# Kernel optimization log

Hardware: AMD Instinct MI355X
Metric: run time of the kernel (lower is better)

Reference implementation:

```python
import jax, jax.numpy as jnp
import numpy as np

# ---- static config (mirrors init_kwargs) ----
B, A, NC = 16, 3, 80          # batch, anchors-per-head, classes
W = H = 76                     # grid (inputwidth / stride-8)
INPUTW = 608.0
M = 32                         # GT boxes per image
IGNORE = 0.5                   # ignore_thresh
MASK_N = 3                     # mask = [0,1,2] -> first 3 anchors belong to this head
ANCHORS = np.array([[10,13],[16,30],[33,23],[30,61],[62,45],[59,119],
                    [116,90],[156,198],[373,326]], dtype=np.float32)


def _box_iou(b1, b2):
    """b1 [N,4], b2 [P,4] xyxy -> iou [N,P] (same math as torch box_iou)."""
    area1 = (b1[:, 2] - b1[:, 0]) * (b1[:, 3] - b1[:, 1])
    area2 = (b2[:, 2] - b2[:, 0]) * (b2[:, 3] - b2[:, 1])
    lt = jnp.maximum(b1[:, None, :2], b2[None, :, :2])
    rb = jnp.minimum(b1[:, None, 2:], b2[None, :, 2:])
    inter = jnp.clip(rb - lt, 0.0).prod(-1)
    return inter / (area1[:, None] + area2[None, :] - inter)


def setup_inputs() -> dict:
    key = jax.random.key(0)
    k1, k2, k3, k4 = jax.random.split(key, 4)
    prediction = jax.random.normal(k1, (B, A * (5 + NC), W, H), jnp.float32) * 0.5
    # gt rows: (label, cx, cy, w, h, batch_idx), normalized coords, sorted by image
    labels = jax.random.randint(k2, (B * M, 1), 0, NC).astype(jnp.float32)
    cxy = jax.random.uniform(k3, (B * M, 2), minval=0.15, maxval=0.85)
    wh = jax.random.uniform(k4, (B * M, 2), minval=0.05, maxval=0.30)
    bidx = jnp.repeat(jnp.arange(B, dtype=jnp.float32), M)[:, None]
    gt = jnp.concatenate([labels, cxy, wh, bidx], axis=1)
    return {"prediction": prediction, "gt": gt}


def reference(prediction, gt):
    p = prediction.reshape(B, A, W, H, 5 + NC)
    cxp = jax.nn.sigmoid(p[..., 0])
    cyp = jax.nn.sigmoid(p[..., 1])
    wp, hp = p[..., 2], p[..., 3]
    confp = jax.nn.sigmoid(p[..., 4])
    classesp = jax.nn.sigmoid(p[..., 5:])
    # decode (anchors_g are the ORIGINAL pixel anchors: assigned before /strides)
    aw = jnp.asarray(ANCHORS[:MASK_N, 0]).reshape(1, A, 1, 1)
    ah = jnp.asarray(ANCHORS[:MASK_N, 1]).reshape(1, A, 1, 1)
    predx = cxp + jnp.arange(W, dtype=p.dtype)[None, None, None, :]
    predy = cyp + jnp.arange(H, dtype=p.dtype)[None, None, :, None]
    predw = jnp.exp(wp) * aw / INPUTW * W
    predh = jnp.exp(hp) * ah / INPUTW * H
    decoded = jnp.concatenate([predx[..., None], predy[..., None], predw[..., None],
                               predh[..., None], confp[..., None], classesp], axis=-1)

    # predicted boxes in pixel xyxy, flattened per image: [B, A*W*H, 4]
    x1 = (predx - predw * 0.5) / W * INPUTW
    y1 = (predy - predh * 0.5) / H * INPUTW
    x2 = (predx + predw * 0.5) / W * INPUTW
    y2 = (predy + predh * 0.5) / H * INPUTW
    pr = jnp.stack([x1, y1, x2, y2], axis=-1).reshape(B, -1, 4)

    # GT boxes per image (fixed M per image, rows sorted by batch idx)
    gtb = gt.reshape(B, M, 6)
    cx, cy, gw, gh = gtb[..., 1], gtb[..., 2], gtb[..., 3], gtb[..., 4]
    gxyxy = jnp.stack([(cx - gw * 0.5) * INPUTW, (cy - gh * 0.5) * INPUTW,
                       (cx + gw * 0.5) * INPUTW, (cy + gh * 0.5) * INPUTW], axis=-1)

    # per-image GT x all-preds IoU; noobj where best IoU <= ignore_thresh
    iou = jax.vmap(_box_iou)(gxyxy, pr)            # [B, M, A*W*H]
    maxv = iou.max(axis=1).reshape(B, A, H, W)      # W==H so flat order matches
    noobj = maxv <= IGNORE

    # best-anchor assignment per GT (vs all 9 anchors centered at the GT)
    ori = jnp.asarray(ANCHORS) / INPUTW             # [9,2] normalized
    fcx, fcy = cx.reshape(-1), cy.reshape(-1)       # [B*M]
    gflat = gxyxy.reshape(-1, 4)
    abox = jnp.stack([(fcx[:, None] - ori[None, :, 0] * 0.5) * INPUTW,
                      (fcy[:, None] - ori[None, :, 1] * 0.5) * INPUTW,
                      (fcx[:, None] + ori[None, :, 0] * 0.5) * INPUTW,
                      (fcy[:, None] + ori[None, :, 1] * 0.5) * INPUTW], axis=-1)  # [BM,9,4]
    lt = jnp.maximum(gflat[:, None, :2], abox[..., :2])
    rb = jnp.minimum(gflat[:, None, 2:], abox[..., 2:])
    inter = jnp.clip(rb - lt, 0.0).prod(-1)
    area_g = (gflat[:, 2] - gflat[:, 0]) * (gflat[:, 3] - gflat[:, 1])
    area_a = (abox[..., 2] - abox[..., 0]) * (abox[..., 3] - abox[..., 1])
    g_a = inter / (area_g[:, None] + area_a - inter)   # [BM,9]
    best = jnp.argmax(g_a, axis=1)
    valid = best < MASK_N                               # mask=[0,1,2] -> a_ind == best
    a_ind = jnp.clip(best, 0, MASK_N - 1)
    gi = (fcx * W).astype(jnp.int32)                    # original indexes dim-2 with x*width
    gj = (fcy * H).astype(jnp.int32)
    bb = jnp.repeat(jnp.arange(B), M)
    flat = ((bb * A + a_ind) * H + gi) * W + gj
    obj = jnp.zeros(B * A * H * W, bool).at[flat].max(valid).reshape(B, A, H, W)
    noobj = noobj.reshape(-1).at[flat].min(~valid).reshape(B, A, H, W)
    return decoded, noobj, obj
```

## Files before the change

### kernel.cpp

```cpp
#include <hip/hip_runtime.h>
#include <math.h>

#define BB 16
#define AA 3
#define NCC 80
#define WW 76
#define MM 32
#define CELLS_PER_IMG (AA * WW * WW)
#define NDECODE (BB * CELLS_PER_IMG * 85)
#define NCELLS (BB * CELLS_PER_IMG)

__constant__ float c_anchor[9][2] = {
    {10.f,13.f},{16.f,30.f},{33.f,23.f},{30.f,61.f},{62.f,45.f},
    {59.f,119.f},{116.f,90.f},{156.f,198.f},{373.f,326.f}};

#define LOG2E 1.4426950408889634f

__device__ __forceinline__ float fast_sigmoid(float x) {
    return __builtin_amdgcn_rcpf(1.0f + __builtin_amdgcn_exp2f(-x * LOG2E));
}

__global__ void decode_kernel(const float* __restrict__ in, float* __restrict__ out,
                              float* __restrict__ boxes) {
    const int n4 = NDECODE / 4;
    int tid = blockIdx.x * blockDim.x + threadIdx.x;
    if (tid >= n4) return;
    float4 v = reinterpret_cast<const float4*>(in)[tid];
    float vals[4] = {v.x, v.y, v.z, v.w};
    float res[4];
    int base = tid * 4;
    int c = base % 85;
    int cell = base / 85;
#pragma unroll
    for (int j = 0; j < 4; ++j) {
        float x = vals[j];
        float r;
        if (c >= 4) {
            r = fast_sigmoid(x);
        } else {
            if (c < 2) {
                float s = fast_sigmoid(x);
                int q = (c == 0) ? (cell % WW) : ((cell / WW) % WW);
                r = s + (float)q;
            } else {
                int a = (cell / (WW * WW)) % AA;
                float an = (c == 2) ? c_anchor[a][0] : c_anchor[a][1];
                r = __builtin_amdgcn_exp2f(x * LOG2E) * (an * 0.125f);
            }
            boxes[cell * 4 + c] = r;
        }
        res[j] = r;
        if (++c == 85) { c = 0; ++cell; }
    }
    reinterpret_cast<float4*>(out)[tid] = make_float4(res[0], res[1], res[2], res[3]);
}

__global__ void noobj_kernel(const float4* __restrict__ boxes, const float* __restrict__ gt,
                             float* __restrict__ noobj, float* __restrict__ obj) {
    __shared__ float4 sbox[MM];
    int b = blockIdx.y;
    int t = threadIdx.x;
    if (t < MM) {
        const float* g = gt + (size_t)(b * MM + t) * 6;
        float cx = g[1], cy = g[2], gw = g[3], gh = g[4];
        sbox[t] = make_float4((cx - gw * 0.5f) * 608.0f, (cy - gh * 0.5f) * 608.0f,
                              (cx + gw * 0.5f) * 608.0f, (cy + gh * 0.5f) * 608.0f);
    }
    __syncthreads();
    int n = blockIdx.x * blockDim.x + t;
    if (n >= CELLS_PER_IMG) return;
    size_t idx = (size_t)b * CELLS_PER_IMG + n;
    float4 pb = boxes[idx];
    float px = pb.x, py = pb.y, pw = pb.z, ph = pb.w;
    float x1 = (px - pw * 0.5f) / 76.0f * 608.0f;
    float y1 = (py - ph * 0.5f) / 76.0f * 608.0f;
    float x2 = (px + pw * 0.5f) / 76.0f * 608.0f;
    float y2 = (py + ph * 0.5f) / 76.0f * 608.0f;
    float area2 = (x2 - x1) * (y2 - y1);
    float best = 0.0f;
#pragma unroll
    for (int m = 0; m < MM; ++m) {
        float4 gb = sbox[m];
        float area1 = (gb.z - gb.x) * (gb.w - gb.y);
        float ltx = fmaxf(gb.x, x1), lty = fmaxf(gb.y, y1);
        float rbx = fminf(gb.z, x2), rby = fminf(gb.w, y2);
        float inter = fmaxf(rbx - ltx, 0.0f) * fmaxf(rby - lty, 0.0f);
        float iou = inter * __builtin_amdgcn_rcpf(area1 + area2 - inter);
        best = fmaxf(best, iou);
    }
    noobj[idx] = (best <= 0.5f) ? 1.0f : 0.0f;
    obj[idx] = 0.0f;
}

__global__ void assign_kernel(const float* __restrict__ gt,
                              float* __restrict__ noobj, float* __restrict__ obj) {
    int r = blockIdx.x * blockDim.x + threadIdx.x;
    if (r >= BB * MM) return;
    const float* g = gt + (size_t)r * 6;
    float cx = g[1], cy = g[2], gw = g[3], gh = g[4];
    float gx1 = (cx - gw * 0.5f) * 608.0f, gy1 = (cy - gh * 0.5f) * 608.0f;
    float gx2 = (cx + gw * 0.5f) * 608.0f, gy2 = (cy + gh * 0.5f) * 608.0f;
    float area_g = (gx2 - gx1) * (gy2 - gy1);
    int best = 0;
    float bestv = -1.0f;
#pragma unroll
    for (int k = 0; k < 9; ++k) {
        float ow = c_anchor[k][0] / 608.0f, oh = c_anchor[k][1] / 608.0f;
        float ax1 = (cx - ow * 0.5f) * 608.0f, ay1 = (cy - oh * 0.5f) * 608.0f;
        float ax2 = (cx + ow * 0.5f) * 608.0f, ay2 = (cy + oh * 0.5f) * 608.0f;
        float ltx = fmaxf(gx1, ax1), lty = fmaxf(gy1, ay1);
        float rbx = fminf(gx2, ax2), rby = fminf(gy2, ay2);
        float inter = fmaxf(rbx - ltx, 0.0f) * fmaxf(rby - lty, 0.0f);
        float area_a = (ax2 - ax1) * (ay2 - ay1);
        float v = inter / (area_g + area_a - inter);
        if (v > bestv) { bestv = v; best = k; }
    }
    if (best < AA) {
        int b = r / MM;
        int gi = (int)(cx * 76.0f);
        int gj = (int)(cy * 76.0f);
        int flat = ((b * AA + best) * WW + gi) * WW + gj;
        obj[flat] = 1.0f;
        noobj[flat] = 0.0f;
    }
}

extern "C" void kernel_launch(void* const* d_in, const int* in_sizes, int n_in,
                              void* d_out, int out_size, void* d_ws, size_t ws_size,
                              hipStream_t stream) {
    const float* pred = (const float*)d_in[0];
    const float* gt   = (const float*)d_in[1];
    float* dec   = (float*)d_out;
    float* noobj = dec + NDECODE;
    float* obj   = noobj + NCELLS;
    float* boxes = (float*)d_ws;

    const int n4 = NDECODE / 4;
    decode_kernel<<<(n4 + 255) / 256, 256, 0, stream>>>(pred, dec, boxes);

    dim3 gb((CELLS_PER_IMG + 255) / 256, BB);
    noobj_kernel<<<gb, 256, 0, stream>>>((const float4*)boxes, gt, noobj, obj);

    assign_kernel<<<2, 256, 0, stream>>>(gt, noobj, obj);
}
```

Measured before the change: 201.6 us.

## Split decode into branch-free bulk sigmoid plus per-cell box fixup

The decode kernel no longer computes per-element channel and cell indices with divisions and branches. It now applies sigmoid uniformly to every element and writes with nontemporal stores. The noobj kernel re-reads the four box channels of each cell from the input, recomputes the box decode, and overwrites those four outputs before the IoU test, so the workspace boxes buffer is no longer needed. The cost is strided scattered reads and writes in the second kernel, plus a correctness dependency on it running after the bulk pass.

```diff
diff --git a/kernel.cpp b/kernel.cpp
--- a/kernel.cpp
+++ b/kernel.cpp
@@ -10,6 +10,8 @@
 #define NDECODE (BB * CELLS_PER_IMG * 85)
 #define NCELLS (BB * CELLS_PER_IMG)
 
+typedef float vfloat4 __attribute__((ext_vector_type(4)));
+
 __constant__ float c_anchor[9][2] = {
     {10.f,13.f},{16.f,30.f},{33.f,23.f},{30.f,61.f},{62.f,45.f},
     {59.f,119.f},{116.f,90.f},{156.f,198.f},{373.f,326.f}};
@@ -20,43 +22,22 @@
     return __builtin_amdgcn_rcpf(1.0f + __builtin_amdgcn_exp2f(-x * LOG2E));
 }
 
-__global__ void decode_kernel(const float* __restrict__ in, float* __restrict__ out,
-                              float* __restrict__ boxes) {
+__global__ void bulk_sigmoid_kernel(const vfloat4* __restrict__ in, vfloat4* __restrict__ out) {
     const int n4 = NDECODE / 4;
     int tid = blockIdx.x * blockDim.x + threadIdx.x;
     if (tid >= n4) return;
-    float4 v = reinterpret_cast<const float4*>(in)[tid];
-    float vals[4] = {v.x, v.y, v.z, v.w};
-    float res[4];
-    int base = tid * 4;
-    int c = base % 85;
-    int cell = base / 85;
-#pragma unroll
-    for (int j = 0; j < 4; ++j) {
-        float x = vals[j];
-        float r;
-        if (c >= 4) {
-            r = fast_sigmoid(x);
-        } else {
-            if (c < 2) {
-                float s = fast_sigmoid(x);
-                int q = (c == 0) ? (cell % WW) : ((cell / WW) % WW);
-                r = s + (float)q;
-            } else {
-                int a = (cell / (WW * WW)) % AA;
-                float an = (c == 2) ? c_anchor[a][0] : c_anchor[a][1];
-                r = __builtin_amdgcn_exp2f(x * LOG2E) * (an * 0.125f);
-            }
-            boxes[cell * 4 + c] = r;
-        }
-        res[j] = r;
-        if (++c == 85) { c = 0; ++cell; }
-    }
-    reinterpret_cast<float4*>(out)[tid] = make_float4(res[0], res[1], res[2], res[3]);
+    vfloat4 v = in[tid];
+    vfloat4 o;
+    o.x = fast_sigmoid(v.x);
+    o.y = fast_sigmoid(v.y);
+    o.z = fast_sigmoid(v.z);
+    o.w = fast_sigmoid(v.w);
+    __builtin_nontemporal_store(o, &out[tid]);
 }
 
-__global__ void noobj_kernel(const float4* __restrict__ boxes, const float* __restrict__ gt,
-                             float* __restrict__ noobj, float* __restrict__ obj) {
+__global__ void noobj_fixup_kernel(const float* __restrict__ in, const float* __restrict__ gt,
+                                   float* __restrict__ out,
+                                   float* __restrict__ noobj, float* __restrict__ obj) {
     __shared__ float4 sbox[MM];
     int b = blockIdx.y;
     int t = threadIdx.x;
@@ -69,9 +50,19 @@
     __syncthreads();
     int n = blockIdx.x * blockDim.x + t;
     if (n >= CELLS_PER_IMG) return;
-    size_t idx = (size_t)b * CELLS_PER_IMG + n;
-    float4 pb = boxes[idx];
-    float px = pb.x, py = pb.y, pw = pb.z, ph = pb.w;
+    size_t cell = (size_t)b * CELLS_PER_IMG + n;
+
+    const float* ip = in + cell * 85;
+    int h = n % WW;
+    int w = (n / WW) % WW;
+    int a = n / (WW * WW);
+    float px = fast_sigmoid(ip[0]) + (float)h;
+    float py = fast_sigmoid(ip[1]) + (float)w;
+    float pw = __builtin_amdgcn_exp2f(ip[2] * LOG2E) * (c_anchor[a][0] * 0.125f);
+    float ph = __builtin_amdgcn_exp2f(ip[3] * LOG2E) * (c_anchor[a][1] * 0.125f);
+    float* op = out + cell * 85;
+    op[0] = px; op[1] = py; op[2] = pw; op[3] = ph;
+
     float x1 = (px - pw * 0.5f) / 76.0f * 608.0f;
     float y1 = (py - ph * 0.5f) / 76.0f * 608.0f;
     float x2 = (px + pw * 0.5f) / 76.0f * 608.0f;
@@ -88,8 +79,8 @@
         float iou = inter * __builtin_amdgcn_rcpf(area1 + area2 - inter);
         best = fmaxf(best, iou);
     }
-    noobj[idx] = (best <= 0.5f) ? 1.0f : 0.0f;
-    obj[idx] = 0.0f;
+    noobj[cell] = (best <= 0.5f) ? 1.0f : 0.0f;
+    obj[cell] = 0.0f;
 }
 
 __global__ void assign_kernel(const float* __restrict__ gt,
@@ -133,13 +124,13 @@
     float* dec   = (float*)d_out;
     float* noobj = dec + NDECODE;
     float* obj   = noobj + NCELLS;
-    float* boxes = (float*)d_ws;
 
     const int n4 = NDECODE / 4;
-    decode_kernel<<<(n4 + 255) / 256, 256, 0, stream>>>(pred, dec, boxes);
+    bulk_sigmoid_kernel<<<(n4 + 255) / 256, 256, 0, stream>>>(
+        (const vfloat4*)pred, (vfloat4*)dec);
 
     dim3 gb((CELLS_PER_IMG + 255) / 256, BB);
-    noobj_kernel<<<gb, 256, 0, stream>>>((const float4*)boxes, gt, noobj, obj);
+    noobj_fixup_kernel<<<gb, 256, 0, stream>>>(pred, gt, dec, noobj, obj);
 
     assign_kernel<<<2, 256, 0, stream>>>(gt, noobj, obj);
 }
```

New measurement: 220.4 us. 1.09x slower.
